# Optimization experiments

Measured on AMD Instinct MI355X. Metric: run time of the kernel, lower is better.

The kernel has to match this reference:

```python
import jax, jax.numpy as jnp
import numpy as np

B, C, N, H, K = 4, 128, 2048, 4, 20
_BN = np.float32(np.sqrt(1.0 + 1e-5))  # eval BatchNorm: running_mean=0, running_var=1


def setup_inputs() -> dict:
    key = jax.random.key(0)
    ks = jax.random.split(key, 16)
    r = lambda k, s: jax.random.normal(k, s, jnp.float32) * 0.1
    u = lambda k, s: jax.random.uniform(k, s, jnp.float32, 0.5, 1.5)
    return {
        "x": jax.random.normal(ks[0], (B, C, N, 1), jnp.float32),
        "fW": r(ks[1], (3, C, C)),
        "fb": r(ks[2], (3, C)),
        "fg": u(ks[3], (3, C)),
        "fbe": r(ks[4], (3, C)),
        "gW1": r(ks[5], (3, C, 2 * C)),
        "gb1": r(ks[6], (3, C)),
        "gg1": u(ks[7], (3, C)),
        "gbe1": r(ks[8], (3, C)),
        "gW2": r(ks[9], (3, C, C)),
        "gb2": r(ks[10], (3, C)),
        "gg2": u(ks[11], (3, C)),
        "gbe2": r(ks[12], (3, C)),
        "pW": r(ks[13], (C, C)),
        "pb": r(ks[14], (C,)),
        "temp": jnp.ones((H, 1, 1), jnp.float32),
        "num_heads": H,
        "k_num": K,
    }


def _filter(x, W, b, g, be):
    # x: [B,C,N]; 1x1 conv -> InstanceNorm(eps=1e-3) -> eval BatchNorm -> ReLU
    y = jnp.einsum('oc,bcn->bon', W, x) + b[:, None]
    m = jnp.mean(y, -1, keepdims=True)
    v = jnp.var(y, -1, keepdims=True)
    y = (y - m) / jnp.sqrt(v + 1e-3)
    return jax.nn.relu(y / _BN * g[:, None] + be[:, None])


def _knn(x, k):
    # x: [B,C,N]; topk of negative squared distance (self included)
    xx = jnp.sum(x * x, axis=1)                     # [B,N]
    inner = jnp.einsum('bcn,bcm->bnm', x, x)        # [B,N,N]
    pd = 2.0 * inner - xx[:, :, None] - xx[:, None, :]
    return jax.lax.top_k(pd, k)[1]                  # [B,N,k]


def _gcn(x, k, W1, b1, g1, be1, W2, b2, g2, be2):
    idx = _knn(x, k)
    xT = jnp.transpose(x, (0, 2, 1))                # [B,N,C]
    nb = jax.vmap(lambda p, i: p[i])(xT, idx)       # [B,N,k,C]
    ctr = jnp.broadcast_to(xT[:, :, None, :], nb.shape)
    feat = jnp.concatenate([ctr, ctr - nb], axis=-1)  # [B,N,k,2C]
    h = jnp.einsum('oi,bnki->bnko', W1, feat) + b1
    h = jax.nn.relu(h / _BN * g1 + be1)
    h = jnp.einsum('oi,bnki->bnko', W2, h) + b2
    h = jax.nn.relu(h / _BN * g2 + be2)
    return jnp.transpose(jnp.max(h, axis=2), (0, 2, 1))  # [B,C,N]


def _l2norm(x):
    n = jnp.sqrt(jnp.sum(x * x, axis=-1, keepdims=True))
    return x / jnp.maximum(n, 1e-12)


def reference(x, fW, fb, fg, fbe, gW1, gb1, gg1, gbe1, gW2, gb2, gg2, gbe2, pW, pb, temp, num_heads, k_num):
    xin = x[..., 0]                                 # [B,C,N]
    Bn, Cc, Nn = xin.shape
    qkv = []
    for i in range(3):  # q, k, v branches (structurally distinct params)
        f = _filter(xin, fW[i], fb[i], fg[i], fbe[i])
        g = _gcn(f, k_num, gW1[i], gb1[i], gg1[i], gbe1[i], gW2[i], gb2[i], gg2[i], gbe2[i])
        qkv.append(g.reshape(Bn, num_heads, Cc // num_heads, Nn))
    q, kk, v = qkv
    q = _l2norm(q)
    kk = _l2norm(kk)
    attn = jnp.einsum('bhcn,bhdn->bhcd', q, kk) * temp  # channel attention [B,H,c,c]
    attn = jax.nn.softmax(attn, axis=-1)
    out = jnp.einsum('bhcd,bhdn->bhcn', attn, v).reshape(Bn, Cc, Nn)
    out = jnp.einsum('oc,bcn->bon', pW, out) + pb[:, None]
    return (out + xin)[..., None]                   # [B,C,N,1]
```

## Files before the change

### kernel.cpp

```cpp
#include <hip/hip_runtime.h>
#include <math.h>


#define B_ 4
#define C_ 128
#define N_ 2048
#define H_ 4
#define K_ 20

typedef __bf16 bf16x8 __attribute__((ext_vector_type(8)));
typedef float f32x4 __attribute__((ext_vector_type(4)));
typedef unsigned int u32x4 __attribute__((ext_vector_type(4)));

__device__ __forceinline__ unsigned short f2bf(float f) {
    unsigned int u = __builtin_bit_cast(unsigned int, f);
    u += 0x7fffu + ((u >> 16) & 1u);
    return (unsigned short)(u >> 16);
}
__device__ __forceinline__ float bf2f(unsigned short s) {
    return __builtin_bit_cast(float, (unsigned int)s << 16);
}

#define PD_STRIDE 4194304
#define OFF_Y     0
#define OFF_P     0
#define OFF_Q     3145728
#define OFF_GT    6291456
#define OFF_AV    9437184
#define OFF_SC    19922944
#define OFF_SH    19924480
#define OFF_XX    19926016
#define OFF_IDX   19950592
#define OFF_G     20442112
#define OFF_NRM   23587840
#define OFF_ATT   23588864

__global__ __launch_bounds__(256) void k_filter_conv(
    const float* __restrict__ x, const float* __restrict__ fW,
    const float* __restrict__ fb, float* __restrict__ y)
{
    __shared__ float Ws[8][C_];
    const int n = blockIdx.x * 256 + threadIdx.x;
    const int o0 = blockIdx.y * 8;
    const int iz = blockIdx.z;
    const int i = iz >> 2, b = iz & 3;
    for (int t = threadIdx.x; t < 8 * C_; t += 256) {
        const int j = t >> 7, c = t & 127;
        Ws[j][c] = fW[((size_t)i * C_ + o0 + j) * C_ + c];
    }
    __syncthreads();
    float acc[8] = {};
    const float* xb = x + ((size_t)b * C_) * N_ + n;
    #pragma unroll 4
    for (int c = 0; c < C_; ++c) {
        const float xv = xb[(size_t)c * N_];
        #pragma unroll
        for (int j = 0; j < 8; ++j) acc[j] += Ws[j][c] * xv;
    }
    float* yb = y + ((size_t)iz * C_ + o0) * N_ + n;
    #pragma unroll
    for (int j = 0; j < 8; ++j) yb[(size_t)j * N_] = acc[j] + fb[i * C_ + o0 + j];
}

__global__ __launch_bounds__(256) void k_rowstats(
    const float* __restrict__ y, const float* __restrict__ fg,
    const float* __restrict__ fbe, float* __restrict__ scale, float* __restrict__ shift)
{
    const int r = blockIdx.x;
    const int i = r >> 9, o = r & 127;
    const float* row = y + (size_t)r * N_;
    float s = 0.f, ss = 0.f;
    for (int n = threadIdx.x; n < N_; n += 256) {
        const float v = row[n];
        s += v; ss += v * v;
    }
    #pragma unroll
    for (int off = 32; off > 0; off >>= 1) {
        s += __shfl_down(s, off);
        ss += __shfl_down(ss, off);
    }
    __shared__ float red[2][4];
    const int wid = threadIdx.x >> 6;
    if ((threadIdx.x & 63) == 0) { red[0][wid] = s; red[1][wid] = ss; }
    __syncthreads();
    if (threadIdx.x == 0) {
        s = red[0][0] + red[0][1] + red[0][2] + red[0][3];
        ss = red[1][0] + red[1][1] + red[1][2] + red[1][3];
        const float mean = s * (1.f / N_);
        const float var = ss * (1.f / N_) - mean * mean;
        const float bn = sqrtf(1.00001f);
        const float sc = fg[i * C_ + o] / (bn * sqrtf(var + 1e-3f));
        scale[r] = sc;
        shift[r] = fbe[i * C_ + o] - mean * sc;
    }
}

__global__ __launch_bounds__(256) void k_norm_transpose(
    const float* __restrict__ y, const float* __restrict__ scale,
    const float* __restrict__ shift,
    unsigned short* __restrict__ fH, unsigned short* __restrict__ fL)
{
    __shared__ float tile[32][33];
    const int n0 = blockIdx.x * 32, o0 = blockIdx.y * 32;
    const int iz = blockIdx.z;
    const int tx = threadIdx.x, ty = threadIdx.y;
    #pragma unroll
    for (int q = 0; q < 4; ++q) {
        const int o = o0 + ty + q * 8;
        const int r = iz * C_ + o;
        const float v = y[(size_t)r * N_ + n0 + tx] * scale[r] + shift[r];
        tile[ty + q * 8][tx] = fmaxf(v, 0.f);
    }
    __syncthreads();
    #pragma unroll
    for (int q = 0; q < 4; ++q) {
        const int n = n0 + ty + q * 8;
        const size_t idx = ((size_t)iz * N_ + n) * C_ + o0 + tx;
        const float v = tile[tx][ty + q * 8];
        const unsigned short hi = f2bf(v);
        fH[idx] = hi;
        fL[idx] = f2bf(v - bf2f(hi));
    }
}

__global__ __launch_bounds__(256) void k_xx(
    const unsigned short* __restrict__ fH, const unsigned short* __restrict__ fL,
    float* __restrict__ xx)
{
    const int r = blockIdx.x * 256 + threadIdx.x;
    const u32x4* rh = (const u32x4*)(fH + (size_t)r * C_);
    const u32x4* rl = (const u32x4*)(fL + (size_t)r * C_);
    float s = 0.f;
    #pragma unroll
    for (int q = 0; q < 16; ++q) {
        const u32x4 hv = rh[q], lv = rl[q];
        #pragma unroll
        for (int e = 0; e < 4; ++e) {
            const unsigned int h = hv[e], l = lv[e];
            const float v0 = bf2f((unsigned short)(h & 0xFFFFu)) + bf2f((unsigned short)(l & 0xFFFFu));
            const float v1 = bf2f((unsigned short)(h >> 16)) + bf2f((unsigned short)(l >> 16));
            s += v0 * v0 + v1 * v1;
        }
    }
    xx[r] = s;
}

__global__ __launch_bounds__(256) void k_pd_mfma(
    const unsigned short* __restrict__ fH, const unsigned short* __restrict__ fL,
    const float* __restrict__ xx, float* __restrict__ pdarena, int ib0)
{
    __shared__ __align__(16) unsigned short Ah[64 * C_], Al[64 * C_];
    __shared__ __align__(16) unsigned short Bh[64 * C_], Bl[64 * C_];
    const int j = blockIdx.z, ib = ib0 + j;
    const unsigned short* fHb = fH + (size_t)ib * N_ * C_;
    const unsigned short* fLb = fL + (size_t)ib * N_ * C_;
    const float* xxb = xx + ib * N_;
    float* pd = pdarena + (size_t)j * PD_STRIDE;
    const int n0 = blockIdx.x * 64, m0 = blockIdx.y * 64;
    const int t = threadIdx.x;
    {
        const int s = t & 15, rb = t >> 4;
        #pragma unroll
        for (int q = 0; q < 4; ++q) {
            const int r = rb + q * 16;
            const int ld = r * 256 + ((s * 16) ^ ((r & 15) << 4));
            *(u32x4*)((char*)Ah + ld) = *(const u32x4*)((const char*)fHb + (size_t)(n0 + r) * 256 + s * 16);
            *(u32x4*)((char*)Al + ld) = *(const u32x4*)((const char*)fLb + (size_t)(n0 + r) * 256 + s * 16);
            *(u32x4*)((char*)Bh + ld) = *(const u32x4*)((const char*)fHb + (size_t)(m0 + r) * 256 + s * 16);
            *(u32x4*)((char*)Bl + ld) = *(const u32x4*)((const char*)fLb + (size_t)(m0 + r) * 256 + s * 16);
        }
    }
    __syncthreads();
    const int lane = t & 63, w = t >> 6;
    const int lr = lane & 15, lg = lane >> 4;
    f32x4 acc[4];
    #pragma unroll
    for (int ct = 0; ct < 4; ++ct) acc[ct] = (f32x4){0.f, 0.f, 0.f, 0.f};
    #pragma unroll
    for (int ks = 0; ks < 4; ++ks) {
        const int arow = w * 16 + lr;
        const int cb = ks * 64 + lg * 16;
        const bf16x8 ah = __builtin_bit_cast(bf16x8,
            *(const u32x4*)((const char*)Ah + arow * 256 + (cb ^ ((arow & 15) << 4))));
        const bf16x8 al = __builtin_bit_cast(bf16x8,
            *(const u32x4*)((const char*)Al + arow * 256 + (cb ^ ((arow & 15) << 4))));
        #pragma unroll
        for (int ct = 0; ct < 4; ++ct) {
            const int brow = ct * 16 + lr;
            const int boff = brow * 256 + (cb ^ ((brow & 15) << 4));
            const bf16x8 bh = __builtin_bit_cast(bf16x8, *(const u32x4*)((const char*)Bh + boff));
            const bf16x8 bl = __builtin_bit_cast(bf16x8, *(const u32x4*)((const char*)Bl + boff));
            acc[ct] = __builtin_amdgcn_mfma_f32_16x16x32_bf16(ah, bh, acc[ct], 0, 0, 0);
            acc[ct] = __builtin_amdgcn_mfma_f32_16x16x32_bf16(ah, bl, acc[ct], 0, 0, 0);
            acc[ct] = __builtin_amdgcn_mfma_f32_16x16x32_bf16(al, bh, acc[ct], 0, 0, 0);
        }
    }
    #pragma unroll
    for (int ct = 0; ct < 4; ++ct) {
        const int m = m0 + ct * 16 + lr;
        const float xm = xxb[m];
        #pragma unroll
        for (int r = 0; r < 4; ++r) {
            const int n = n0 + w * 16 + lg * 4 + r;
            pd[(size_t)n * N_ + m] = 2.f * acc[ct][r] - xxb[n] - xm;
        }
    }
}

__global__ __launch_bounds__(256) void k_topk(
    const float* __restrict__ pdarena, int* __restrict__ idxb, int ib0)
{
    const int j = blockIdx.y;
    const float* pd = pdarena + (size_t)j * PD_STRIDE;
    const int lane = threadIdx.x & 63;
    const int n = blockIdx.x * 4 + (threadIdx.x >> 6);
    int* out = idxb + ((size_t)(ib0 + j) * N_ + n) * K_;
    const float* row = pd + (size_t)n * N_;
    float v[32];
    #pragma unroll
    for (int jj = 0; jj < 32; ++jj) v[jj] = row[jj * 64 + lane];
    for (int it = 0; it < K_; ++it) {
        float best = -3e38f; int bj = 0;
        #pragma unroll
        for (int jj = 0; jj < 32; ++jj) if (v[jj] > best) { best = v[jj]; bj = jj; }
        int bm = bj * 64 + lane;
        #pragma unroll
        for (int off = 1; off < 64; off <<= 1) {
            const float ov = __shfl_xor(best, off);
            const int   om = __shfl_xor(bm, off);
            if (ov > best || (ov == best && om < bm)) { best = ov; bm = om; }
        }
        if (lane == 0) out[it] = bm;
        if ((bm & 63) == lane) {
            const int jc = bm >> 6;
            #pragma unroll
            for (int jj = 0; jj < 32; ++jj) if (jj == jc) v[jj] = -3e38f;
        }
    }
}

__global__ __launch_bounds__(256) void k_pq_mfma(
    const unsigned short* __restrict__ fH, const unsigned short* __restrict__ fL,
    const float* __restrict__ gW1, float* __restrict__ P, float* __restrict__ Q)
{
    __shared__ __align__(16) unsigned short Ah[64 * C_], Al[64 * C_];
    __shared__ __align__(16) unsigned short Bh[64 * C_], Bl[64 * C_];
    const int iz = blockIdx.z, i = iz >> 2;
    const int n0 = blockIdx.x * 64;
    const int yt = blockIdx.y;
    const bool isQ = (yt >= 2);
    const int oc0 = (yt & 1) * 64;
    const int t = threadIdx.x;
    const unsigned short* fHb = fH + (size_t)iz * N_ * C_;
    const unsigned short* fLb = fL + (size_t)iz * N_ * C_;
    {
        const int s = t & 15, rb = t >> 4;
        #pragma unroll
        for (int q = 0; q < 4; ++q) {
            const int r = rb + q * 16;
            const int ld = r * 256 + ((s * 16) ^ ((r & 15) << 4));
            *(u32x4*)((char*)Ah + ld) = *(const u32x4*)((const char*)fHb + (size_t)(n0 + r) * 256 + s * 16);
            *(u32x4*)((char*)Al + ld) = *(const u32x4*)((const char*)fLb + (size_t)(n0 + r) * 256 + s * 16);
        }
    }
    {
        const int cs = t & 15, ro = t >> 4;
        #pragma unroll
        for (int q = 0; q < 4; ++q) {
            const int o = ro + q * 16;
            const float* wrow = gW1 + ((size_t)i * C_ + oc0 + o) * (2 * C_) + cs * 8;
            const float4 a0 = *(const float4*)(wrow);
            const float4 a1 = *(const float4*)(wrow + 4);
            const float4 b0 = *(const float4*)(wrow + C_);
            const float4 b1 = *(const float4*)(wrow + C_ + 4);
            float cmb[8];
            if (isQ) {
                cmb[0] = -b0.x; cmb[1] = -b0.y; cmb[2] = -b0.z; cmb[3] = -b0.w;
                cmb[4] = -b1.x; cmb[5] = -b1.y; cmb[6] = -b1.z; cmb[7] = -b1.w;
            } else {
                cmb[0] = a0.x + b0.x; cmb[1] = a0.y + b0.y; cmb[2] = a0.z + b0.z; cmb[3] = a0.w + b0.w;
                cmb[4] = a1.x + b1.x; cmb[5] = a1.y + b1.y; cmb[6] = a1.z + b1.z; cmb[7] = a1.w + b1.w;
            }
            unsigned int ph[4], pl[4];
            #pragma unroll
            for (int e = 0; e < 4; ++e) {
                const unsigned short h0 = f2bf(cmb[e * 2 + 0]);
                const unsigned short h1 = f2bf(cmb[e * 2 + 1]);
                const unsigned short l0 = f2bf(cmb[e * 2 + 0] - bf2f(h0));
                const unsigned short l1 = f2bf(cmb[e * 2 + 1] - bf2f(h1));
                ph[e] = (unsigned int)h0 | ((unsigned int)h1 << 16);
                pl[e] = (unsigned int)l0 | ((unsigned int)l1 << 16);
            }
            const int ld = o * 256 + ((cs * 16) ^ ((o & 15) << 4));
            *(u32x4*)((char*)Bh + ld) = (u32x4){ph[0], ph[1], ph[2], ph[3]};
            *(u32x4*)((char*)Bl + ld) = (u32x4){pl[0], pl[1], pl[2], pl[3]};
        }
    }
    __syncthreads();
    const int lane = t & 63, w = t >> 6;
    const int lr = lane & 15, lg = lane >> 4;
    f32x4 acc[4];
    #pragma unroll
    for (int ct = 0; ct < 4; ++ct) acc[ct] = (f32x4){0.f, 0.f, 0.f, 0.f};
    #pragma unroll
    for (int ks = 0; ks < 4; ++ks) {
        const int arow = w * 16 + lr;
        const int cb = ks * 64 + lg * 16;
        const bf16x8 ah = __builtin_bit_cast(bf16x8,
            *(const u32x4*)((const char*)Ah + arow * 256 + (cb ^ ((arow & 15) << 4))));
        const bf16x8 al = __builtin_bit_cast(bf16x8,
            *(const u32x4*)((const char*)Al + arow * 256 + (cb ^ ((arow & 15) << 4))));
        #pragma unroll
        for (int ct = 0; ct < 4; ++ct) {
            const int brow = ct * 16 + lr;
            const int boff = brow * 256 + (cb ^ ((brow & 15) << 4));
            const bf16x8 bh = __builtin_bit_cast(bf16x8, *(const u32x4*)((const char*)Bh + boff));
            const bf16x8 bl = __builtin_bit_cast(bf16x8, *(const u32x4*)((const char*)Bl + boff));
            acc[ct] = __builtin_amdgcn_mfma_f32_16x16x32_bf16(ah, bh, acc[ct], 0, 0, 0);
            acc[ct] = __builtin_amdgcn_mfma_f32_16x16x32_bf16(ah, bl, acc[ct], 0, 0, 0);
            acc[ct] = __builtin_amdgcn_mfma_f32_16x16x32_bf16(al, bh, acc[ct], 0, 0, 0);
        }
    }
    float* outp = (isQ ? Q : P) + (size_t)iz * N_ * C_;
    #pragma unroll
    for (int ct = 0; ct < 4; ++ct) {
        #pragma unroll
        for (int r = 0; r < 4; ++r) {
            const int n = n0 + w * 16 + lg * 4 + r;
            outp[(size_t)n * C_ + oc0 + ct * 16 + lr] = acc[ct][r];
        }
    }
}

__global__ __launch_bounds__(256) void k_edge2(
    const float* __restrict__ P, const float* __restrict__ Q, const int* __restrict__ idxb,
    const float* __restrict__ gb1, const float* __restrict__ gg1, const float* __restrict__ gbe1,
    const float* __restrict__ gW2, const float* __restrict__ gb2, const float* __restrict__ gg2,
    const float* __restrict__ gbe2, float* __restrict__ gT)
{
    __shared__ __align__(16) unsigned short h1s[160 * C_];
    __shared__ __align__(16) unsigned short W2s[C_ * C_];
    __shared__ float s1s[C_], t1s[C_], s2s[C_], t2s[C_];
    __shared__ int idxs[160];
    const int i = blockIdx.z, b = blockIdx.y;
    const int p0 = blockIdx.x * 8;
    const int t = threadIdx.x;
    const size_t base = (size_t)(i * B_ + b) * N_;

    if (t < C_) {
        const float bn = sqrtf(1.00001f);
        const float g1 = gg1[i * C_ + t];
        s1s[t] = g1 / bn;
        t1s[t] = gb1[i * C_ + t] * (g1 / bn) + gbe1[i * C_ + t];
        const float g2 = gg2[i * C_ + t];
        s2s[t] = g2 / bn;
        t2s[t] = gb2[i * C_ + t] * (g2 / bn) + gbe2[i * C_ + t];
    }
    if (t < 160) idxs[t] = idxb[base * K_ + p0 * K_ + t];
    __syncthreads();

    const int seg = t & 7;
    const int rb = t >> 3;
    float4 s1v[4], t1v[4];
    #pragma unroll
    for (int q = 0; q < 4; ++q) {
        s1v[q] = *(const float4*)&s1s[seg * 16 + q * 4];
        t1v[q] = *(const float4*)&t1s[seg * 16 + q * 4];
    }
    const float* Pb = P + base * C_;
    const float* Qb = Q + base * C_;
    #pragma unroll
    for (int it = 0; it < 5; ++it) {
        const int row = rb + 32 * it;
        const int p = row / 20;
        const int m = idxs[row];
        const float* Pr = Pb + (size_t)(p0 + p) * C_ + seg * 16;
        const float* Qr = Qb + (size_t)m * C_ + seg * 16;
        unsigned int pk[8];
        #pragma unroll
        for (int q = 0; q < 4; ++q) {
            const float4 pv = *(const float4*)(Pr + q * 4);
            const float4 qv = *(const float4*)(Qr + q * 4);
            const float r0 = fmaxf((pv.x + qv.x) * s1v[q].x + t1v[q].x, 0.f);
            const float r1 = fmaxf((pv.y + qv.y) * s1v[q].y + t1v[q].y, 0.f);
            const float r2 = fmaxf((pv.z + qv.z) * s1v[q].z + t1v[q].z, 0.f);
            const float r3 = fmaxf((pv.w + qv.w) * s1v[q].w + t1v[q].w, 0.f);
            pk[q * 2 + 0] = (unsigned int)f2bf(r0) | ((unsigned int)f2bf(r1) << 16);
            pk[q * 2 + 1] = (unsigned int)f2bf(r2) | ((unsigned int)f2bf(r3) << 16);
        }
        const int sw = (row & 15) << 4;
        char* bp = (char*)h1s + row * 256;
        *(u32x4*)(bp + ((seg * 32) ^ sw))      = (u32x4){pk[0], pk[1], pk[2], pk[3]};
        *(u32x4*)(bp + ((seg * 32 + 16) ^ sw)) = (u32x4){pk[4], pk[5], pk[6], pk[7]};
    }
    #pragma unroll
    for (int it = 0; it < 4; ++it) {
        const int o = rb + 32 * it;
        const float* wr = gW2 + ((size_t)i * C_ + o) * C_ + seg * 16;
        unsigned int pk[8];
        #pragma unroll
        for (int q = 0; q < 4; ++q) {
            const float4 wv = *(const float4*)(wr + q * 4);
            pk[q * 2 + 0] = (unsigned int)f2bf(wv.x) | ((unsigned int)f2bf(wv.y) << 16);
            pk[q * 2 + 1] = (unsigned int)f2bf(wv.z) | ((unsigned int)f2bf(wv.w) << 16);
        }
        const int sw = (o & 15) << 4;
        char* bp = (char*)W2s + o * 256;
        *(u32x4*)(bp + ((seg * 32) ^ sw))      = (u32x4){pk[0], pk[1], pk[2], pk[3]};
        *(u32x4*)(bp + ((seg * 32 + 16) ^ sw)) = (u32x4){pk[4], pk[5], pk[6], pk[7]};
    }
    __syncthreads();

    const int lane = t & 63, w = t >> 6;
    const int lr = lane & 15, lg = lane >> 4;
    bf16x8 Bf[2][4];
    #pragma unroll
    for (int nb = 0; nb < 2; ++nb)
        #pragma unroll
        for (int ks = 0; ks < 4; ++ks) {
            const int o = w * 32 + nb * 16 + lr;
            const int cb = ks * 64 + lg * 16;
            Bf[nb][ks] = __builtin_bit_cast(bf16x8,
                *(const u32x4*)((const char*)W2s + o * 256 + (cb ^ ((o & 15) << 4))));
        }
    f32x4 acc[10][2];
    #pragma unroll
    for (int mt = 0; mt < 10; ++mt)
        #pragma unroll
        for (int nb = 0; nb < 2; ++nb)
            acc[mt][nb] = (f32x4){0.f, 0.f, 0.f, 0.f};
    #pragma unroll
    for (int mt = 0; mt < 10; ++mt) {
        bf16x8 Af[4];
        #pragma unroll
        for (int ks = 0; ks < 4; ++ks) {
            const int row = mt * 16 + lr;
            const int cb = ks * 64 + lg * 16;
            Af[ks] = __builtin_bit_cast(bf16x8,
                *(const u32x4*)((const char*)h1s + row * 256 + (cb ^ ((row & 15) << 4))));
        }
        #pragma unroll
        for (int nb = 0; nb < 2; ++nb)
            #pragma unroll
            for (int ks = 0; ks < 4; ++ks)
                acc[mt][nb] = __builtin_amdgcn_mfma_f32_16x16x32_bf16(
                    Af[ks], Bf[nb][ks], acc[mt][nb], 0, 0, 0);
    }
    __syncthreads();

    #pragma unroll
    for (int mt = 0; mt < 10; ++mt)
        #pragma unroll
        for (int nb = 0; nb < 2; ++nb) {
            const int col = w * 32 + nb * 16 + lr;
            const float s2c = s2s[col], t2c = t2s[col];
            #pragma unroll
            for (int r = 0; r < 4; ++r) {
                const int row = mt * 16 + lg * 4 + r;
                const float v = fmaxf(acc[mt][nb][r] * s2c + t2c, 0.f);
                *(unsigned short*)((char*)h1s + row * 256 + ((col * 2) ^ ((row & 15) << 4))) = f2bf(v);
            }
        }
    __syncthreads();

    const int oc = t & 127, ph = t >> 7;
    float* gp = gT + (base + p0) * C_;
    #pragma unroll
    for (int pp = 0; pp < 4; ++pp) {
        const int p = ph * 4 + pp;
        float mx = 0.f;
        #pragma unroll
        for (int j = 0; j < 20; ++j) {
            const int row = p * 20 + j;
            const unsigned short us =
                *(const unsigned short*)((const char*)h1s + row * 256 + ((oc * 2) ^ ((row & 15) << 4)));
            mx = fmaxf(mx, bf2f(us));
        }
        gp[(size_t)p * C_ + oc] = mx;
    }
}

__global__ __launch_bounds__(256) void k_transpose2(
    const float* __restrict__ gT, float* __restrict__ g)
{
    __shared__ float tile[32][33];
    const int n0 = blockIdx.x * 32, o0 = blockIdx.y * 32;
    const int iz = blockIdx.z;
    const int tx = threadIdx.x, ty = threadIdx.y;
    #pragma unroll
    for (int q = 0; q < 4; ++q) {
        const int n = n0 + ty + q * 8;
        tile[ty + q * 8][tx] = gT[((size_t)iz * N_ + n) * C_ + o0 + tx];
    }
    __syncthreads();
    #pragma unroll
    for (int q = 0; q < 4; ++q) {
        const int o = o0 + ty + q * 8;
        g[((size_t)iz * C_ + o) * N_ + n0 + tx] = tile[tx][ty + q * 8];
    }
}

__global__ __launch_bounds__(256) void k_l2norm(const float* __restrict__ g, float* __restrict__ norms)
{
    const int r = blockIdx.x;
    const float* row = g + (size_t)r * N_;
    float s = 0.f;
    for (int n = threadIdx.x; n < N_; n += 256) { const float v = row[n]; s += v * v; }
    #pragma unroll
    for (int off = 32; off > 0; off >>= 1) s += __shfl_down(s, off);
    __shared__ float red[4];
    if ((threadIdx.x & 63) == 0) red[threadIdx.x >> 6] = s;
    __syncthreads();
    if (threadIdx.x == 0)
        norms[r] = fmaxf(sqrtf(red[0] + red[1] + red[2] + red[3]), 1e-12f);
}

__global__ __launch_bounds__(256) void k_attn(
    const float* __restrict__ g, const float* __restrict__ norms,
    const float* __restrict__ temp, float* __restrict__ attn)
{
    __shared__ float qs[N_];
    __shared__ float rowv[32];
    const int r = blockIdx.x;
    const int c = r & 31, h = (r >> 5) & 3, b = r >> 7;
    const float* qrow  = g + ((size_t)(0 * B_ + b) * C_ + h * 32 + c) * N_;
    const float* krows = g + ((size_t)(1 * B_ + b) * C_ + h * 32) * N_;
    for (int n = threadIdx.x; n < N_; n += 256) qs[n] = qrow[n];
    __syncthreads();
    const int d = threadIdx.x >> 3, s = threadIdx.x & 7;
    const float* kr = krows + (size_t)d * N_;
    float acc = 0.f;
    for (int m = 0; m < N_ / 32; ++m) {
        const int n = (m * 8 + s) * 4;
        const float4 kv = *(const float4*)(kr + n);
        acc += qs[n] * kv.x + qs[n+1] * kv.y + qs[n+2] * kv.z + qs[n+3] * kv.w;
    }
    #pragma unroll
    for (int off = 1; off < 8; off <<= 1) acc += __shfl_xor(acc, off);
    if (s == 0) rowv[d] = acc;
    __syncthreads();
    if (threadIdx.x < 32) {
        const int dd = threadIdx.x;
        const float nq = norms[(size_t)(0 * B_ + b) * C_ + h * 32 + c];
        const float nk = norms[(size_t)(1 * B_ + b) * C_ + h * 32 + dd];
        const float v = rowv[dd] / (nq * nk) * temp[h];
        float mx = v;
        #pragma unroll
        for (int off = 1; off < 32; off <<= 1) mx = fmaxf(mx, __shfl_xor(mx, off));
        const float e = expf(v - mx);
        float sm = e;
        #pragma unroll
        for (int off = 1; off < 32; off <<= 1) sm += __shfl_xor(sm, off);
        attn[(size_t)r * 32 + dd] = e / sm;
    }
}

__global__ __launch_bounds__(256) void k_av(
    const float* __restrict__ attn, const float* __restrict__ g, float* __restrict__ av)
{
    __shared__ float at[32][32];
    const int n = blockIdx.x * 256 + threadIdx.x;
    const int h = blockIdx.y, b = blockIdx.z;
    for (int t2 = threadIdx.x; t2 < 1024; t2 += 256)
        at[t2 >> 5][t2 & 31] = attn[((size_t)(b * H_ + h)) * 1024 + t2];
    __syncthreads();
    const float* vrows = g + ((size_t)(2 * B_ + b) * C_ + h * 32) * N_;
    float acc[32] = {};
    for (int dd = 0; dd < 32; ++dd) {
        const float vv = vrows[(size_t)dd * N_ + n];
        #pragma unroll
        for (int cc = 0; cc < 32; ++cc) acc[cc] += at[cc][dd] * vv;
    }
    float* avb = av + ((size_t)b * C_ + h * 32) * N_ + n;
    #pragma unroll
    for (int cc = 0; cc < 32; ++cc) avb[(size_t)cc * N_] = acc[cc];
}

__global__ __launch_bounds__(256) void k_proj(
    const float* __restrict__ av, const float* __restrict__ pW, const float* __restrict__ pb,
    const float* __restrict__ x, float* __restrict__ out)
{
    __shared__ float Ws[8][C_];
    const int n = blockIdx.x * 256 + threadIdx.x;
    const int o0 = blockIdx.y * 8;
    const int b = blockIdx.z;
    for (int t = threadIdx.x; t < 8 * C_; t += 256) {
        const int j = t >> 7, c = t & 127;
        Ws[j][c] = pW[(size_t)(o0 + j) * C_ + c];
    }
    __syncthreads();
    float acc[8] = {};
    const float* ab = av + ((size_t)b * C_) * N_ + n;
    #pragma unroll 4
    for (int c = 0; c < C_; ++c) {
        const float vv = ab[(size_t)c * N_];
        #pragma unroll
        for (int j = 0; j < 8; ++j) acc[j] += Ws[j][c] * vv;
    }
    #pragma unroll
    for (int j = 0; j < 8; ++j) {
        const int o = o0 + j;
        const size_t off = ((size_t)b * C_ + o) * N_ + n;
        out[off] = acc[j] + pb[o] + x[off];
    }
}

extern "C" void kernel_launch(void* const* d_in, const int* in_sizes, int n_in,
                              void* d_out, int out_size, void* d_ws, size_t ws_size,
                              hipStream_t stream)
{
    const float* x    = (const float*)d_in[0];
    const float* fW   = (const float*)d_in[1];
    const float* fb   = (const float*)d_in[2];
    const float* fg   = (const float*)d_in[3];
    const float* fbe  = (const float*)d_in[4];
    const float* gW1  = (const float*)d_in[5];
    const float* gb1  = (const float*)d_in[6];
    const float* gg1  = (const float*)d_in[7];
    const float* gbe1 = (const float*)d_in[8];
    const float* gW2  = (const float*)d_in[9];
    const float* gb2  = (const float*)d_in[10];
    const float* gg2  = (const float*)d_in[11];
    const float* gbe2 = (const float*)d_in[12];
    const float* pW   = (const float*)d_in[13];
    const float* pb   = (const float*)d_in[14];
    const float* temp = (const float*)d_in[15];
    float* ws = (float*)d_ws;

    float* arena = ws;
    float* y    = ws + OFF_Y;
    float* P    = ws + OFF_P;
    float* Q    = ws + OFF_Q;
    float* gT   = ws + OFF_GT;
    float* av   = ws + OFF_AV;
    float* sc   = ws + OFF_SC;
    float* sh   = ws + OFF_SH;
    float* xx   = ws + OFF_XX;
    int*   idxb = (int*)(ws + OFF_IDX);
    float* g    = ws + OFF_G;
    float* nrm  = ws + OFF_NRM;
    float* attn = ws + OFF_ATT;
    unsigned short* fH = (unsigned short*)g;
    unsigned short* fL = fH + (size_t)12 * N_ * C_;

    k_filter_conv<<<dim3(N_/256, C_/8, 12), 256, 0, stream>>>(x, fW, fb, y);
    k_rowstats<<<12 * C_, 256, 0, stream>>>(y, fg, fbe, sc, sh);
    k_norm_transpose<<<dim3(N_/32, C_/32, 12), dim3(32, 8), 0, stream>>>(y, sc, sh, fH, fL);
    k_xx<<<(12 * N_) / 256, 256, 0, stream>>>(fH, fL, xx);
    for (int g4 = 0; g4 < 3; ++g4) {
        k_pd_mfma<<<dim3(N_/64, N_/64, 4), 256, 0, stream>>>(fH, fL, xx, arena, g4 * 4);
        k_topk<<<dim3(N_/4, 4), 256, 0, stream>>>(arena, idxb, g4 * 4);
    }
    k_pq_mfma<<<dim3(N_/64, 4, 12), 256, 0, stream>>>(fH, fL, gW1, P, Q);
    k_edge2<<<dim3(N_/8, B_, 3), 256, 0, stream>>>(P, Q, idxb, gb1, gg1, gbe1,
                                                   gW2, gb2, gg2, gbe2, gT);
    k_transpose2<<<dim3(N_/32, C_/32, 12), dim3(32, 8), 0, stream>>>(gT, g);
    k_l2norm<<<2 * B_ * C_, 256, 0, stream>>>(g, nrm);
    k_attn<<<B_ * H_ * 32, 256, 0, stream>>>(g, nrm, temp, attn);
    k_av<<<dim3(N_/256, H_, B_), 256, 0, stream>>>(attn, g, av);
    k_proj<<<dim3(N_/256, C_/8, B_), 256, 0, stream>>>(av, pW, pb, x, (float*)d_out);
    (void)in_sizes; (void)n_in; (void)out_size; (void)ws_size;
}
```

Before: 499.8 us.

## Precompute bf16 edge-conv weights and store P/Q as pre-scaled bf16

Adds a small prep kernel that converts gW2 (with the BN2 scale folded in) and the combined P/Q halves of gW1 to bf16 hi/lo once. The pq kernel then loads these directly instead of converting per block, applies the BN1 scale/shift in its epilogue, and writes P and Q as bf16 instead of fp32. The edge kernel reads bf16 P/Q and W2 fragments straight from global memory, which drops the W2 shared-memory staging and allows a 3-blocks-per-CU launch bound. This targets the conversion work repeated in every block and halves P/Q gather traffic, at the cost of extra rounding on P and Q before they are summed.

```diff
diff --git a/kernel.cpp b/kernel.cpp
--- a/kernel.cpp
+++ b/kernel.cpp
@@ -20,11 +20,17 @@
 __device__ __forceinline__ float bf2f(unsigned short s) {
     return __builtin_bit_cast(float, (unsigned int)s << 16);
 }
+__device__ __forceinline__ float bflo(unsigned int u) {
+    return __builtin_bit_cast(float, u << 16);
+}
+__device__ __forceinline__ float bfhi(unsigned int u) {
+    return __builtin_bit_cast(float, u & 0xFFFF0000u);
+}
 
 #define PD_STRIDE 4194304
 #define OFF_Y     0
 #define OFF_P     0
-#define OFF_Q     3145728
+#define OFF_Q     1572864
 #define OFF_GT    6291456
 #define OFF_AV    9437184
 #define OFF_SC    19922944
@@ -34,6 +40,11 @@
 #define OFF_G     20442112
 #define OFF_NRM   23587840
 #define OFF_ATT   23588864
+#define OFF_W2B   23605248
+#define OFF_PWH   23629824
+#define OFF_PWL   23654400
+#define OFF_QWH   23678976
+#define OFF_QWL   23703552
 
 __global__ __launch_bounds__(256) void k_filter_conv(
     const float* __restrict__ x, const float* __restrict__ fW,
@@ -60,6 +71,50 @@
     float* yb = y + ((size_t)iz * C_ + o0) * N_ + n;
     #pragma unroll
     for (int j = 0; j < 8; ++j) yb[(size_t)j * N_] = acc[j] + fb[i * C_ + o0 + j];
+}
+
+__global__ __launch_bounds__(256) void k_prep(
+    const float* __restrict__ gW2, const float* __restrict__ gg2,
+    const float* __restrict__ gW1,
+    unsigned short* __restrict__ W2b,
+    unsigned short* __restrict__ PWh, unsigned short* __restrict__ PWl,
+    unsigned short* __restrict__ QWh, unsigned short* __restrict__ QWl)
+{
+    const int i = blockIdx.x;
+    const float bn = sqrtf(1.00001f);
+    for (int id = threadIdx.x; id < 4096; id += 256) {
+        const int o = id >> 5, c4 = (id & 31) * 4;
+        const size_t eo = (size_t)i * C_ * C_ + o * C_ + c4;
+        {
+            const float s2 = gg2[i * C_ + o] / bn;
+            const float4 wv = *(const float4*)(gW2 + ((size_t)i * C_ + o) * C_ + c4);
+            uint2 pk;
+            pk.x = (unsigned int)f2bf(wv.x * s2) | ((unsigned int)f2bf(wv.y * s2) << 16);
+            pk.y = (unsigned int)f2bf(wv.z * s2) | ((unsigned int)f2bf(wv.w * s2) << 16);
+            *(uint2*)(W2b + eo) = pk;
+        }
+        {
+            const float* wrow = gW1 + ((size_t)i * C_ + o) * (2 * C_);
+            const float4 wa = *(const float4*)(wrow + c4);
+            const float4 wb = *(const float4*)(wrow + C_ + c4);
+            const float pv[4] = {wa.x + wb.x, wa.y + wb.y, wa.z + wb.z, wa.w + wb.w};
+            const float qv[4] = {-wb.x, -wb.y, -wb.z, -wb.w};
+            unsigned short ph[4], pl[4], qh[4], ql[4];
+            #pragma unroll
+            for (int e = 0; e < 4; ++e) {
+                ph[e] = f2bf(pv[e]); pl[e] = f2bf(pv[e] - bf2f(ph[e]));
+                qh[e] = f2bf(qv[e]); ql[e] = f2bf(qv[e] - bf2f(qh[e]));
+            }
+            *(uint2*)(PWh + eo) = (uint2){(unsigned int)ph[0] | ((unsigned int)ph[1] << 16),
+                                          (unsigned int)ph[2] | ((unsigned int)ph[3] << 16)};
+            *(uint2*)(PWl + eo) = (uint2){(unsigned int)pl[0] | ((unsigned int)pl[1] << 16),
+                                          (unsigned int)pl[2] | ((unsigned int)pl[3] << 16)};
+            *(uint2*)(QWh + eo) = (uint2){(unsigned int)qh[0] | ((unsigned int)qh[1] << 16),
+                                          (unsigned int)qh[2] | ((unsigned int)qh[3] << 16)};
+            *(uint2*)(QWl + eo) = (uint2){(unsigned int)ql[0] | ((unsigned int)ql[1] << 16),
+                                          (unsigned int)ql[2] | ((unsigned int)ql[3] << 16)};
+        }
+    }
 }
 
 __global__ __launch_bounds__(256) void k_rowstats(
@@ -136,9 +191,8 @@
         const u32x4 hv = rh[q], lv = rl[q];
         #pragma unroll
         for (int e = 0; e < 4; ++e) {
-            const unsigned int h = hv[e], l = lv[e];
-            const float v0 = bf2f((unsigned short)(h & 0xFFFFu)) + bf2f((unsigned short)(l & 0xFFFFu));
-            const float v1 = bf2f((unsigned short)(h >> 16)) + bf2f((unsigned short)(l >> 16));
+            const float v0 = bflo(hv[e]) + bflo(lv[e]);
+            const float v1 = bfhi(hv[e]) + bfhi(lv[e]);
             s += v0 * v0 + v1 * v1;
         }
     }
@@ -241,7 +295,11 @@
 
 __global__ __launch_bounds__(256) void k_pq_mfma(
     const unsigned short* __restrict__ fH, const unsigned short* __restrict__ fL,
-    const float* __restrict__ gW1, float* __restrict__ P, float* __restrict__ Q)
+    const unsigned short* __restrict__ PWh, const unsigned short* __restrict__ PWl,
+    const unsigned short* __restrict__ QWh, const unsigned short* __restrict__ QWl,
+    const float* __restrict__ gg1, const float* __restrict__ gb1,
+    const float* __restrict__ gbe1,
+    unsigned short* __restrict__ Pb, unsigned short* __restrict__ Qb)
 {
     __shared__ __align__(16) unsigned short Ah[64 * C_], Al[64 * C_];
     __shared__ __align__(16) unsigned short Bh[64 * C_], Bl[64 * C_];
@@ -253,6 +311,8 @@
     const int t = threadIdx.x;
     const unsigned short* fHb = fH + (size_t)iz * N_ * C_;
     const unsigned short* fLb = fL + (size_t)iz * N_ * C_;
+    const unsigned short* Wh = (isQ ? QWh : PWh) + (size_t)i * C_ * C_;
+    const unsigned short* Wl = (isQ ? QWl : PWl) + (size_t)i * C_ * C_;
     {
         const int s = t & 15, rb = t >> 4;
         #pragma unroll
@@ -261,39 +321,8 @@
             const int ld = r * 256 + ((s * 16) ^ ((r & 15) << 4));
             *(u32x4*)((char*)Ah + ld) = *(const u32x4*)((const char*)fHb + (size_t)(n0 + r) * 256 + s * 16);
             *(u32x4*)((char*)Al + ld) = *(const u32x4*)((const char*)fLb + (size_t)(n0 + r) * 256 + s * 16);
-        }
-    }
-    {
-        const int cs = t & 15, ro = t >> 4;
-        #pragma unroll
-        for (int q = 0; q < 4; ++q) {
-            const int o = ro + q * 16;
-            const float* wrow = gW1 + ((size_t)i * C_ + oc0 + o) * (2 * C_) + cs * 8;
-            const float4 a0 = *(const float4*)(wrow);
-            const float4 a1 = *(const float4*)(wrow + 4);
-            const float4 b0 = *(const float4*)(wrow + C_);
-            const float4 b1 = *(const float4*)(wrow + C_ + 4);
-            float cmb[8];
-            if (isQ) {
-                cmb[0] = -b0.x; cmb[1] = -b0.y; cmb[2] = -b0.z; cmb[3] = -b0.w;
-                cmb[4] = -b1.x; cmb[5] = -b1.y; cmb[6] = -b1.z; cmb[7] = -b1.w;
-            } else {
-                cmb[0] = a0.x + b0.x; cmb[1] = a0.y + b0.y; cmb[2] = a0.z + b0.z; cmb[3] = a0.w + b0.w;
-                cmb[4] = a1.x + b1.x; cmb[5] = a1.y + b1.y; cmb[6] = a1.z + b1.z; cmb[7] = a1.w + b1.w;
-            }
-            unsigned int ph[4], pl[4];
-            #pragma unroll
-            for (int e = 0; e < 4; ++e) {
-                const unsigned short h0 = f2bf(cmb[e * 2 + 0]);
-                const unsigned short h1 = f2bf(cmb[e * 2 + 1]);
-                const unsigned short l0 = f2bf(cmb[e * 2 + 0] - bf2f(h0));
-                const unsigned short l1 = f2bf(cmb[e * 2 + 1] - bf2f(h1));
-                ph[e] = (unsigned int)h0 | ((unsigned int)h1 << 16);
-                pl[e] = (unsigned int)l0 | ((unsigned int)l1 << 16);
-            }
-            const int ld = o * 256 + ((cs * 16) ^ ((o & 15) << 4));
-            *(u32x4*)((char*)Bh + ld) = (u32x4){ph[0], ph[1], ph[2], ph[3]};
-            *(u32x4*)((char*)Bl + ld) = (u32x4){pl[0], pl[1], pl[2], pl[3]};
+            *(u32x4*)((char*)Bh + ld) = *(const u32x4*)((const char*)(Wh + (size_t)(oc0 + r) * C_) + s * 16);
+            *(u32x4*)((char*)Bl + ld) = *(const u32x4*)((const char*)(Wl + (size_t)(oc0 + r) * C_) + s * 16);
         }
     }
     __syncthreads();
@@ -321,26 +350,29 @@
             acc[ct] = __builtin_amdgcn_mfma_f32_16x16x32_bf16(al, bh, acc[ct], 0, 0, 0);
         }
     }
-    float* outp = (isQ ? Q : P) + (size_t)iz * N_ * C_;
+    const float bn = sqrtf(1.00001f);
+    unsigned short* outp = (isQ ? Qb : Pb) + (size_t)iz * N_ * C_;
     #pragma unroll
     for (int ct = 0; ct < 4; ++ct) {
+        const int col = oc0 + ct * 16 + lr;
+        const float s1 = gg1[i * C_ + col] / bn;
+        const float t1 = isQ ? 0.f : (gb1[i * C_ + col] * s1 + gbe1[i * C_ + col]);
         #pragma unroll
         for (int r = 0; r < 4; ++r) {
             const int n = n0 + w * 16 + lg * 4 + r;
-            outp[(size_t)n * C_ + oc0 + ct * 16 + lr] = acc[ct][r];
-        }
-    }
-}
-
-__global__ __launch_bounds__(256) void k_edge2(
-    const float* __restrict__ P, const float* __restrict__ Q, const int* __restrict__ idxb,
-    const float* __restrict__ gb1, const float* __restrict__ gg1, const float* __restrict__ gbe1,
-    const float* __restrict__ gW2, const float* __restrict__ gb2, const float* __restrict__ gg2,
+            outp[(size_t)n * C_ + col] = f2bf(acc[ct][r] * s1 + t1);
+        }
+    }
+}
+
+__global__ __launch_bounds__(256, 3) void k_edge2(
+    const unsigned short* __restrict__ Pb, const unsigned short* __restrict__ Qb,
+    const int* __restrict__ idxb, const unsigned short* __restrict__ W2b,
+    const float* __restrict__ gg2, const float* __restrict__ gb2,
     const float* __restrict__ gbe2, float* __restrict__ gT)
 {
     __shared__ __align__(16) unsigned short h1s[160 * C_];
-    __shared__ __align__(16) unsigned short W2s[C_ * C_];
-    __shared__ float s1s[C_], t1s[C_], s2s[C_], t2s[C_];
+    __shared__ float t2s[C_];
     __shared__ int idxs[160];
     const int i = blockIdx.z, b = blockIdx.y;
     const int p0 = blockIdx.x * 8;
@@ -349,80 +381,55 @@
 
     if (t < C_) {
         const float bn = sqrtf(1.00001f);
-        const float g1 = gg1[i * C_ + t];
-        s1s[t] = g1 / bn;
-        t1s[t] = gb1[i * C_ + t] * (g1 / bn) + gbe1[i * C_ + t];
-        const float g2 = gg2[i * C_ + t];
-        s2s[t] = g2 / bn;
-        t2s[t] = gb2[i * C_ + t] * (g2 / bn) + gbe2[i * C_ + t];
+        const float s2 = gg2[i * C_ + t] / bn;
+        t2s[t] = gb2[i * C_ + t] * s2 + gbe2[i * C_ + t];
     }
     if (t < 160) idxs[t] = idxb[base * K_ + p0 * K_ + t];
     __syncthreads();
+
+    const int lane = t & 63, w = t >> 6;
+    const int lr = lane & 15, lg = lane >> 4;
+    const unsigned short* W2bi = W2b + (size_t)i * C_ * C_;
+    bf16x8 Bf[2][4];
+    #pragma unroll
+    for (int nb = 0; nb < 2; ++nb)
+        #pragma unroll
+        for (int ks = 0; ks < 4; ++ks) {
+            const int o = w * 32 + nb * 16 + lr;
+            Bf[nb][ks] = __builtin_bit_cast(bf16x8,
+                *(const u32x4*)(W2bi + (size_t)o * C_ + ks * 32 + lg * 8));
+        }
 
     const int seg = t & 7;
     const int rb = t >> 3;
-    float4 s1v[4], t1v[4];
-    #pragma unroll
-    for (int q = 0; q < 4; ++q) {
-        s1v[q] = *(const float4*)&s1s[seg * 16 + q * 4];
-        t1v[q] = *(const float4*)&t1s[seg * 16 + q * 4];
-    }
-    const float* Pb = P + base * C_;
-    const float* Qb = Q + base * C_;
+    const unsigned short* Pr0 = Pb + base * C_;
+    const unsigned short* Qr0 = Qb + base * C_;
     #pragma unroll
     for (int it = 0; it < 5; ++it) {
         const int row = rb + 32 * it;
         const int p = row / 20;
         const int m = idxs[row];
-        const float* Pr = Pb + (size_t)(p0 + p) * C_ + seg * 16;
-        const float* Qr = Qb + (size_t)m * C_ + seg * 16;
+        const u32x4* Pr = (const u32x4*)(Pr0 + (size_t)(p0 + p) * C_ + seg * 16);
+        const u32x4* Qr = (const u32x4*)(Qr0 + (size_t)m * C_ + seg * 16);
+        const u32x4 pv0 = Pr[0], pv1 = Pr[1];
+        const u32x4 qv0 = Qr[0], qv1 = Qr[1];
         unsigned int pk[8];
         #pragma unroll
-        for (int q = 0; q < 4; ++q) {
-            const float4 pv = *(const float4*)(Pr + q * 4);
-            const float4 qv = *(const float4*)(Qr + q * 4);
-            const float r0 = fmaxf((pv.x + qv.x) * s1v[q].x + t1v[q].x, 0.f);
-            const float r1 = fmaxf((pv.y + qv.y) * s1v[q].y + t1v[q].y, 0.f);
-            const float r2 = fmaxf((pv.z + qv.z) * s1v[q].z + t1v[q].z, 0.f);
-            const float r3 = fmaxf((pv.w + qv.w) * s1v[q].w + t1v[q].w, 0.f);
-            pk[q * 2 + 0] = (unsigned int)f2bf(r0) | ((unsigned int)f2bf(r1) << 16);
-            pk[q * 2 + 1] = (unsigned int)f2bf(r2) | ((unsigned int)f2bf(r3) << 16);
+        for (int e = 0; e < 4; ++e) {
+            const float lo0 = fmaxf(bflo(pv0[e]) + bflo(qv0[e]), 0.f);
+            const float hi0 = fmaxf(bfhi(pv0[e]) + bfhi(qv0[e]), 0.f);
+            pk[e] = (unsigned int)f2bf(lo0) | ((unsigned int)f2bf(hi0) << 16);
+            const float lo1 = fmaxf(bflo(pv1[e]) + bflo(qv1[e]), 0.f);
+            const float hi1 = fmaxf(bfhi(pv1[e]) + bfhi(qv1[e]), 0.f);
+            pk[e + 4] = (unsigned int)f2bf(lo1) | ((unsigned int)f2bf(hi1) << 16);
         }
         const int sw = (row & 15) << 4;
         char* bp = (char*)h1s + row * 256;
         *(u32x4*)(bp + ((seg * 32) ^ sw))      = (u32x4){pk[0], pk[1], pk[2], pk[3]};
         *(u32x4*)(bp + ((seg * 32 + 16) ^ sw)) = (u32x4){pk[4], pk[5], pk[6], pk[7]};
     }
-    #pragma unroll
-    for (int it = 0; it < 4; ++it) {
-        const int o = rb + 32 * it;
-        const float* wr = gW2 + ((size_t)i * C_ + o) * C_ + seg * 16;
-        unsigned int pk[8];
-        #pragma unroll
-        for (int q = 0; q < 4; ++q) {
-            const float4 wv = *(const float4*)(wr + q * 4);
-            pk[q * 2 + 0] = (unsigned int)f2bf(wv.x) | ((unsigned int)f2bf(wv.y) << 16);
-            pk[q * 2 + 1] = (unsigned int)f2bf(wv.z) | ((unsigned int)f2bf(wv.w) << 16);
-        }
-        const int sw = (o & 15) << 4;
-        char* bp = (char*)W2s + o * 256;
-        *(u32x4*)(bp + ((seg * 32) ^ sw))      = (u32x4){pk[0], pk[1], pk[2], pk[3]};
-        *(u32x4*)(bp + ((seg * 32 + 16) ^ sw)) = (u32x4){pk[4], pk[5], pk[6], pk[7]};
-    }
-    __syncthreads();
-
-    const int lane = t & 63, w = t >> 6;
-    const int lr = lane & 15, lg = lane >> 4;
-    bf16x8 Bf[2][4];
-    #pragma unroll
-    for (int nb = 0; nb < 2; ++nb)
-        #pragma unroll
-        for (int ks = 0; ks < 4; ++ks) {
-            const int o = w * 32 + nb * 16 + lr;
-            const int cb = ks * 64 + lg * 16;
-            Bf[nb][ks] = __builtin_bit_cast(bf16x8,
-                *(const u32x4*)((const char*)W2s + o * 256 + (cb ^ ((o & 15) << 4))));
-        }
+    __syncthreads();
+
     f32x4 acc[10][2];
     #pragma unroll
     for (int mt = 0; mt < 10; ++mt)
@@ -453,11 +460,11 @@
         #pragma unroll
         for (int nb = 0; nb < 2; ++nb) {
             const int col = w * 32 + nb * 16 + lr;
-            const float s2c = s2s[col], t2c = t2s[col];
+            const float t2c = t2s[col];
             #pragma unroll
             for (int r = 0; r < 4; ++r) {
                 const int row = mt * 16 + lg * 4 + r;
-                const float v = fmaxf(acc[mt][nb][r] * s2c + t2c, 0.f);
+                const float v = fmaxf(acc[mt][nb][r] + t2c, 0.f);
                 *(unsigned short*)((char*)h1s + row * 256 + ((col * 2) ^ ((row & 15) << 4))) = f2bf(v);
             }
         }
@@ -629,8 +636,8 @@
 
     float* arena = ws;
     float* y    = ws + OFF_Y;
-    float* P    = ws + OFF_P;
-    float* Q    = ws + OFF_Q;
+    unsigned short* Pb = (unsigned short*)(ws + OFF_P);
+    unsigned short* Qb = (unsigned short*)(ws + OFF_Q);
     float* gT   = ws + OFF_GT;
     float* av   = ws + OFF_AV;
     float* sc   = ws + OFF_SC;
@@ -640,10 +647,16 @@
     float* g    = ws + OFF_G;
     float* nrm  = ws + OFF_NRM;
     float* attn = ws + OFF_ATT;
+    unsigned short* W2b = (unsigned short*)(ws + OFF_W2B);
+    unsigned short* PWh = (unsigned short*)(ws + OFF_PWH);
+    unsigned short* PWl = (unsigned short*)(ws + OFF_PWL);
+    unsigned short* QWh = (unsigned short*)(ws + OFF_QWH);
+    unsigned short* QWl = (unsigned short*)(ws + OFF_QWL);
     unsigned short* fH = (unsigned short*)g;
     unsigned short* fL = fH + (size_t)12 * N_ * C_;
 
     k_filter_conv<<<dim3(N_/256, C_/8, 12), 256, 0, stream>>>(x, fW, fb, y);
+    k_prep<<<3, 256, 0, stream>>>(gW2, gg2, gW1, W2b, PWh, PWl, QWh, QWl);
     k_rowstats<<<12 * C_, 256, 0, stream>>>(y, fg, fbe, sc, sh);
     k_norm_transpose<<<dim3(N_/32, C_/32, 12), dim3(32, 8), 0, stream>>>(y, sc, sh, fH, fL);
     k_xx<<<(12 * N_) / 256, 256, 0, stream>>>(fH, fL, xx);
@@ -651,9 +664,10 @@
         k_pd_mfma<<<dim3(N_/64, N_/64, 4), 256, 0, stream>>>(fH, fL, xx, arena, g4 * 4);
         k_topk<<<dim3(N_/4, 4), 256, 0, stream>>>(arena, idxb, g4 * 4);
     }
-    k_pq_mfma<<<dim3(N_/64, 4, 12), 256, 0, stream>>>(fH, fL, gW1, P, Q);
-    k_edge2<<<dim3(N_/8, B_, 3), 256, 0, stream>>>(P, Q, idxb, gb1, gg1, gbe1,
-                                                   gW2, gb2, gg2, gbe2, gT);
+    k_pq_mfma<<<dim3(N_/64, 4, 12), 256, 0, stream>>>(fH, fL, PWh, PWl, QWh, QWl,
+                                                      gg1, gb1, gbe1, Pb, Qb);
+    k_edge2<<<dim3(N_/8, B_, 3), 256, 0, stream>>>(Pb, Qb, idxb, W2b,
+                                                   gg2, gb2, gbe2, gT);
     k_transpose2<<<dim3(N_/32, C_/32, 12), dim3(32, 8), 0, stream>>>(gT, g);
     k_l2norm<<<2 * B_ * C_, 256, 0, stream>>>(g, nrm);
     k_attn<<<B_ * H_ * 32, 256, 0, stream>>>(g, nrm, temp, attn);
```

New measurement: 489.4 us. -2.1%, faster.
